# Performance work log

Measured on AMD Instinct MI355X. Metric: run time of the kernel, lower is better.

## Reference

```python
import jax, jax.numpy as jnp
import numpy as np

B, S, D, U, A = 8, 2048, 1024, 1024, 4  # batch, seq, input_dim, units, n_activations


def setup_inputs() -> dict:
    key = jax.random.key(0)
    ks = jax.random.split(key, 6)
    scale_w = (6.0 / (D + U)) ** 0.5  # glorot_uniform
    scale_wf = (6.0 / (U + A)) ** 0.5
    scale_wa = (6.0 / (D + A)) ** 0.5
    return {
        "x": jax.random.normal(ks[0], (B, S, D), dtype=jnp.float32),
        "w": jax.random.uniform(ks[1], (D, U), jnp.float32, -scale_w, scale_w),
        "b": jnp.zeros((U,), jnp.float32),
        "wf": jax.random.uniform(ks[2], (U, A), jnp.float32, -scale_wf, scale_wf),
        "bf": jnp.zeros((U, A), jnp.float32),
        "w_att": jax.random.uniform(ks[3], (D, A), jnp.float32, -scale_wa, scale_wa),
        "b_att": jnp.zeros((A,), jnp.float32),
    }


def reference(x, w, b, wf, bf, w_att, b_att):
    # weighted_sum: [B,S,U]
    ws = jnp.einsum('bsd,du->bsu', x, w) + b
    # broadcast per-activation affine: [B,S,U,A]
    wa = ws[..., None] * wf + bf
    acts = [
        jax.nn.relu(wa[..., 0]),
        jax.nn.sigmoid(wa[..., 1]),
        jnp.tanh(wa[..., 2]),
        jax.nn.gelu(wa[..., 3], approximate=False),  # tf.nn.gelu default is exact
    ]
    result_activations = jnp.stack(acts, axis=-1)  # [B,S,U,A]
    # attention over activations: [B,S,A]
    attn = jax.nn.softmax(jnp.einsum('bsd,da->bsa', x, w_att) + b_att, axis=-1)
    # weighted reduce over activation axis -> [B,S,U]
    out = jnp.einsum('bsua,bsa->bsu', result_activations, attn)
    return out
```

## Files before the change

kernel.cpp:

```cpp
#include <hip/hip_runtime.h>
#include <hip/hip_bf16.h>
#include <cstdint>

#define B_ 8
#define S_ 2048
#define D_ 1024
#define U_ 1024
#define M_ (B_ * S_)

typedef __bf16 bf16x8 __attribute__((ext_vector_type(8)));
typedef float  f32x4  __attribute__((ext_vector_type(4)));

__device__ __forceinline__ uint16_t f2bf(float f) {
  uint32_t u = __builtin_bit_cast(uint32_t, f);
  u += 0x7fffu + ((u >> 16) & 1u);
  return (uint16_t)(u >> 16);
}

__device__ __forceinline__ void async_copy16(const void* g, void* l) {
  typedef const __attribute__((address_space(1))) uint8_t* gp_t;
  typedef __attribute__((address_space(3))) uint8_t* lp_t;
  __builtin_amdgcn_global_load_lds((gp_t)(uintptr_t)g,
                                   (lp_t)(uint32_t)(uintptr_t)l, 16, 0, 0);
}

__global__ __launch_bounds__(256) void k_prep(
    const float* __restrict__ x, const float* __restrict__ w_att,
    const float* __restrict__ b_att, const float* __restrict__ w,
    uint16_t* __restrict__ x_bf, float* __restrict__ attn,
    uint16_t* __restrict__ wt) {
  __shared__ float tile[32][33];
  const int bid = blockIdx.x;
  if (bid < M_ / 4) {
    const int wave = threadIdx.x >> 6, lane = threadIdx.x & 63;
    const int row = bid * 4 + wave;
    const float4* xr = reinterpret_cast<const float4*>(x + (size_t)row * D_);
    const float4* wa4 = reinterpret_cast<const float4*>(w_att);
    float4 v[4];
#pragma unroll
    for (int i = 0; i < 4; i++) v[i] = xr[lane + 64 * i];
    float4 p = {0.f, 0.f, 0.f, 0.f};
#pragma unroll
    for (int i = 0; i < 4; i++) {
      const int base = 4 * (lane + 64 * i);
      const float xe[4] = {v[i].x, v[i].y, v[i].z, v[i].w};
#pragma unroll
      for (int c = 0; c < 4; c++) {
        float4 wv = wa4[base + c];
        p.x = fmaf(xe[c], wv.x, p.x);
        p.y = fmaf(xe[c], wv.y, p.y);
        p.z = fmaf(xe[c], wv.z, p.z);
        p.w = fmaf(xe[c], wv.w, p.w);
      }
      ushort4 hb;
      hb.x = f2bf(v[i].x); hb.y = f2bf(v[i].y);
      hb.z = f2bf(v[i].z); hb.w = f2bf(v[i].w);
      reinterpret_cast<ushort4*>(x_bf + (size_t)row * D_)[lane + 64 * i] = hb;
    }
#pragma unroll
    for (int off = 32; off > 0; off >>= 1) {
      p.x += __shfl_xor(p.x, off);
      p.y += __shfl_xor(p.y, off);
      p.z += __shfl_xor(p.z, off);
      p.w += __shfl_xor(p.w, off);
    }
    if (lane == 0) {
      float l0 = p.x + b_att[0], l1 = p.y + b_att[1];
      float l2 = p.z + b_att[2], l3 = p.w + b_att[3];
      float mx = fmaxf(fmaxf(l0, l1), fmaxf(l2, l3));
      float e0 = __expf(l0 - mx), e1 = __expf(l1 - mx);
      float e2 = __expf(l2 - mx), e3 = __expf(l3 - mx);
      float inv = __builtin_amdgcn_rcpf(e0 + e1 + e2 + e3);
      reinterpret_cast<float4*>(attn)[row] =
          make_float4(e0 * inv, e1 * inv, e2 * inv, e3 * inv);
    }
  } else {
    const int wid = bid - M_ / 4;
    const int t = threadIdx.x;
    const int tx = t & 31, ty = t >> 5;
    const int c0 = (wid & 31) * 32;
    const int r0 = (wid >> 5) * 32;
#pragma unroll
    for (int i = 0; i < 4; i++) {
      int r = ty + i * 8;
      tile[r][tx] = w[(size_t)(r0 + r) * U_ + c0 + tx];
    }
    __syncthreads();
#pragma unroll
    for (int i = 0; i < 4; i++) {
      int r = ty + i * 8;
      wt[(size_t)(c0 + r) * D_ + r0 + tx] = f2bf(tile[tx][r]);
    }
  }
}

#define BM 128
#define BN 128
#define BK 64
#define NXB (U_ / BN)
#define NWG ((M_ / BM) * NXB)

__global__ __launch_bounds__(256, 4) void k_gemm_ep(
    const uint16_t* __restrict__ xbf, const uint16_t* __restrict__ wt,
    const float* __restrict__ bias, const float* __restrict__ wf,
    const float* __restrict__ bfb, const float* __restrict__ attn,
    float* __restrict__ out) {
  __shared__ uint16_t As[BM * BK];
  __shared__ uint16_t Bs[BN * BK];

  const int t = threadIdx.x;
  const int wave = t >> 6, lane = t & 63;
  const int l16 = lane & 15, quad = lane >> 4;
  const int wm = wave >> 1, wn = wave & 1;

  const int h = blockIdx.y * NXB + blockIdx.x;
  const int l = (h & 7) * (NWG / 8) + (h >> 3);
  const int bx = l & (NXB - 1);
  const int by = l / NXB;
  const int m0 = by * BM;
  const int n0 = bx * BN;

  const uint16_t* aBase = xbf + (size_t)m0 * D_;
  const uint16_t* bBase = wt + (size_t)n0 * D_;

  f32x4 acc[4][4] = {};

  for (int k0 = 0; k0 < D_; k0 += BK) {
#pragma unroll
    for (int it = 0; it < 4; it++) {
      int c = t + it * 256;
      int r = c >> 3;
      int cs = c & 7;
      int gc = cs ^ (r & 7);
      async_copy16(aBase + (size_t)r * D_ + k0 + gc * 8, (uint8_t*)As + c * 16);
      async_copy16(bBase + (size_t)r * D_ + k0 + gc * 8, (uint8_t*)Bs + c * 16);
    }
    __syncthreads();

#pragma unroll
    for (int ks = 0; ks < 2; ks++) {
      const int kcb = ks * 4;
      bf16x8 af[4], bfr[4];
#pragma unroll
      for (int i = 0; i < 4; i++) {
        int r = wm * 64 + i * 16 + l16;
        int cs = (kcb + quad) ^ (r & 7);
        af[i] = *reinterpret_cast<const bf16x8*>(&As[r * BK + cs * 8]);
      }
#pragma unroll
      for (int j = 0; j < 4; j++) {
        int n = wn * 64 + j * 16 + l16;
        int cs = (kcb + quad) ^ (n & 7);
        bfr[j] = *reinterpret_cast<const bf16x8*>(&Bs[n * BK + cs * 8]);
      }
#pragma unroll
      for (int i = 0; i < 4; i++)
#pragma unroll
        for (int j = 0; j < 4; j++)
          acc[i][j] = __builtin_amdgcn_mfma_f32_16x16x32_bf16(af[i], bfr[j], acc[i][j], 0, 0, 0);
    }
    __syncthreads();
  }

  float bu[4];
  float4 wf4[4], bf4[4];
#pragma unroll
  for (int j = 0; j < 4; j++) {
    int u = n0 + wn * 64 + j * 16 + l16;
    bu[j] = bias[u];
    wf4[j] = reinterpret_cast<const float4*>(wf)[u];
    bf4[j] = reinterpret_cast<const float4*>(bfb)[u];
  }
#pragma unroll
  for (int i = 0; i < 4; i++) {
#pragma unroll
    for (int r = 0; r < 4; r++) {
      int mg = m0 + wm * 64 + i * 16 + quad * 4 + r;
      float4 at = reinterpret_cast<const float4*>(attn)[mg];
      float* orow = out + (size_t)mg * U_;
#pragma unroll
      for (int j = 0; j < 4; j++) {
        int u = n0 + wn * 64 + j * 16 + l16;
        float wsv = acc[i][j][r] + bu[j];
        float wa0 = fmaf(wsv, wf4[j].x, bf4[j].x);
        float wa1 = fmaf(wsv, wf4[j].y, bf4[j].y);
        float wa2 = fmaf(wsv, wf4[j].z, bf4[j].z);
        float wa3 = fmaf(wsv, wf4[j].w, bf4[j].w);
        float a_relu = fmaxf(wa0, 0.f);
        float a_sig = __builtin_amdgcn_rcpf(
            1.f + __builtin_amdgcn_exp2f(-1.4426950409f * wa1));
        float a_tanh = fmaf(2.f, __builtin_amdgcn_rcpf(
            1.f + __builtin_amdgcn_exp2f(-2.8853900818f * wa2)), -1.f);
        float y = wa3 * fmaf(0.044715f, wa3 * wa3, 1.f);
        float a_gelu = wa3 * __builtin_amdgcn_rcpf(
            1.f + __builtin_amdgcn_exp2f(-2.302207929f * y));
        float res = at.x * a_relu + at.y * a_sig + at.z * a_tanh + at.w * a_gelu;
        __builtin_nontemporal_store(res, &orow[u]);
      }
    }
  }
}

extern "C" void kernel_launch(void* const* d_in, const int* in_sizes, int n_in,
                              void* d_out, int out_size, void* d_ws, size_t ws_size,
                              hipStream_t stream) {
  const float* x     = (const float*)d_in[0];
  const float* w     = (const float*)d_in[1];
  const float* b     = (const float*)d_in[2];
  const float* wf    = (const float*)d_in[3];
  const float* bfb   = (const float*)d_in[4];
  const float* w_att = (const float*)d_in[5];
  const float* b_att = (const float*)d_in[6];
  float* out = (float*)d_out;

  char* ws = (char*)d_ws;
  uint16_t* x_bf = (uint16_t*)ws;
  uint16_t* w_t  = (uint16_t*)(ws + ((size_t)32 << 20));
  float*    attn = (float*)(ws + ((size_t)34 << 20));

  k_prep<<<dim3(M_ / 4 + 1024), 256, 0, stream>>>(x, w_att, b_att, w, x_bf, attn, w_t);
  k_gemm_ep<<<dim3(U_ / BN, M_ / BM), 256, 0, stream>>>(x_bf, w_t, b, wf, bfb, attn, out);
}
```

Before: 173.8 us.

## Fuse x bf16 conversion and attention logits into GEMM A-tile loads

Drops the prep pass that wrote a bf16 copy of x and the attention softmax to workspace. The GEMM now loads fp32 x directly, converts it to bf16 in registers before storing to LDS, and accumulates the attention logits during the k-loop, finishing the softmax in shared memory. This removes a full read/write pass over x and one kernel's worth of traffic. In exchange, each of the 8 column blocks re-reads fp32 x (twice the bytes of bf16), the A loads become synchronous instead of async-to-LDS, and the attention dot product is recomputed once per column block. The output store is also changed from nontemporal to a normal store.

```diff
diff --git a/kernel.cpp b/kernel.cpp
--- a/kernel.cpp
+++ b/kernel.cpp
@@ -24,73 +24,24 @@
                                    (lp_t)(uint32_t)(uintptr_t)l, 16, 0, 0);
 }
 
-__global__ __launch_bounds__(256) void k_prep(
-    const float* __restrict__ x, const float* __restrict__ w_att,
-    const float* __restrict__ b_att, const float* __restrict__ w,
-    uint16_t* __restrict__ x_bf, float* __restrict__ attn,
-    uint16_t* __restrict__ wt) {
+__global__ __launch_bounds__(256) void k_tr(
+    const float* __restrict__ w, uint16_t* __restrict__ wt) {
   __shared__ float tile[32][33];
-  const int bid = blockIdx.x;
-  if (bid < M_ / 4) {
-    const int wave = threadIdx.x >> 6, lane = threadIdx.x & 63;
-    const int row = bid * 4 + wave;
-    const float4* xr = reinterpret_cast<const float4*>(x + (size_t)row * D_);
-    const float4* wa4 = reinterpret_cast<const float4*>(w_att);
-    float4 v[4];
-#pragma unroll
-    for (int i = 0; i < 4; i++) v[i] = xr[lane + 64 * i];
-    float4 p = {0.f, 0.f, 0.f, 0.f};
-#pragma unroll
-    for (int i = 0; i < 4; i++) {
-      const int base = 4 * (lane + 64 * i);
-      const float xe[4] = {v[i].x, v[i].y, v[i].z, v[i].w};
-#pragma unroll
-      for (int c = 0; c < 4; c++) {
-        float4 wv = wa4[base + c];
-        p.x = fmaf(xe[c], wv.x, p.x);
-        p.y = fmaf(xe[c], wv.y, p.y);
-        p.z = fmaf(xe[c], wv.z, p.z);
-        p.w = fmaf(xe[c], wv.w, p.w);
-      }
-      ushort4 hb;
-      hb.x = f2bf(v[i].x); hb.y = f2bf(v[i].y);
-      hb.z = f2bf(v[i].z); hb.w = f2bf(v[i].w);
-      reinterpret_cast<ushort4*>(x_bf + (size_t)row * D_)[lane + 64 * i] = hb;
-    }
-#pragma unroll
-    for (int off = 32; off > 0; off >>= 1) {
-      p.x += __shfl_xor(p.x, off);
-      p.y += __shfl_xor(p.y, off);
-      p.z += __shfl_xor(p.z, off);
-      p.w += __shfl_xor(p.w, off);
-    }
-    if (lane == 0) {
-      float l0 = p.x + b_att[0], l1 = p.y + b_att[1];
-      float l2 = p.z + b_att[2], l3 = p.w + b_att[3];
-      float mx = fmaxf(fmaxf(l0, l1), fmaxf(l2, l3));
-      float e0 = __expf(l0 - mx), e1 = __expf(l1 - mx);
-      float e2 = __expf(l2 - mx), e3 = __expf(l3 - mx);
-      float inv = __builtin_amdgcn_rcpf(e0 + e1 + e2 + e3);
-      reinterpret_cast<float4*>(attn)[row] =
-          make_float4(e0 * inv, e1 * inv, e2 * inv, e3 * inv);
-    }
-  } else {
-    const int wid = bid - M_ / 4;
-    const int t = threadIdx.x;
-    const int tx = t & 31, ty = t >> 5;
-    const int c0 = (wid & 31) * 32;
-    const int r0 = (wid >> 5) * 32;
-#pragma unroll
-    for (int i = 0; i < 4; i++) {
-      int r = ty + i * 8;
-      tile[r][tx] = w[(size_t)(r0 + r) * U_ + c0 + tx];
-    }
-    __syncthreads();
-#pragma unroll
-    for (int i = 0; i < 4; i++) {
-      int r = ty + i * 8;
-      wt[(size_t)(c0 + r) * D_ + r0 + tx] = f2bf(tile[tx][r]);
-    }
+  const int wid = blockIdx.x;
+  const int t = threadIdx.x;
+  const int tx = t & 31, ty = t >> 5;
+  const int c0 = (wid & 31) * 32;
+  const int r0 = (wid >> 5) * 32;
+#pragma unroll
+  for (int i = 0; i < 4; i++) {
+    int r = ty + i * 8;
+    tile[r][tx] = w[(size_t)(r0 + r) * U_ + c0 + tx];
+  }
+  __syncthreads();
+#pragma unroll
+  for (int i = 0; i < 4; i++) {
+    int r = ty + i * 8;
+    wt[(size_t)(c0 + r) * D_ + r0 + tx] = f2bf(tile[tx][r]);
   }
 }
 
@@ -100,13 +51,14 @@
 #define NXB (U_ / BN)
 #define NWG ((M_ / BM) * NXB)
 
-__global__ __launch_bounds__(256, 4) void k_gemm_ep(
-    const uint16_t* __restrict__ xbf, const uint16_t* __restrict__ wt,
+__global__ __launch_bounds__(256, 4) void k_gemm_f(
+    const float* __restrict__ x, const uint16_t* __restrict__ wt,
     const float* __restrict__ bias, const float* __restrict__ wf,
-    const float* __restrict__ bfb, const float* __restrict__ attn,
-    float* __restrict__ out) {
+    const float* __restrict__ bfb, const float* __restrict__ w_att,
+    const float* __restrict__ b_att, float* __restrict__ out) {
   __shared__ uint16_t As[BM * BK];
   __shared__ uint16_t Bs[BN * BK];
+  __shared__ float4 attn_s[BM];
 
   const int t = threadIdx.x;
   const int wave = t >> 6, lane = t & 63;
@@ -120,20 +72,45 @@
   const int m0 = by * BM;
   const int n0 = bx * BN;
 
-  const uint16_t* aBase = xbf + (size_t)m0 * D_;
   const uint16_t* bBase = wt + (size_t)n0 * D_;
+  const float4* wa4 = reinterpret_cast<const float4*>(w_att);
 
   f32x4 acc[4][4] = {};
+  float4 patt[4] = {};
 
   for (int k0 = 0; k0 < D_; k0 += BK) {
 #pragma unroll
     for (int it = 0; it < 4; it++) {
       int c = t + it * 256;
       int r = c >> 3;
-      int cs = c & 7;
-      int gc = cs ^ (r & 7);
-      async_copy16(aBase + (size_t)r * D_ + k0 + gc * 8, (uint8_t*)As + c * 16);
+      int gc = (c & 7) ^ (r & 7);
       async_copy16(bBase + (size_t)r * D_ + k0 + gc * 8, (uint8_t*)Bs + c * 16);
+    }
+#pragma unroll
+    for (int it = 0; it < 4; it++) {
+      int c = t + it * 256;
+      int r = c >> 3;
+      int gc = (c & 7) ^ (r & 7);
+      const float* g = x + (size_t)(m0 + r) * D_ + k0 + gc * 8;
+      float4 lo = *reinterpret_cast<const float4*>(g);
+      float4 hi = *reinterpret_cast<const float4*>(g + 4);
+      const float4* wrow = wa4 + k0 + gc * 8;
+      float4 pa = patt[it];
+#define ACC4(val, wv) do { float4 _w = (wv);                        \
+        pa.x = fmaf((val), _w.x, pa.x); pa.y = fmaf((val), _w.y, pa.y); \
+        pa.z = fmaf((val), _w.z, pa.z); pa.w = fmaf((val), _w.w, pa.w); } while (0)
+      ACC4(lo.x, wrow[0]); ACC4(lo.y, wrow[1]);
+      ACC4(lo.z, wrow[2]); ACC4(lo.w, wrow[3]);
+      ACC4(hi.x, wrow[4]); ACC4(hi.y, wrow[5]);
+      ACC4(hi.z, wrow[6]); ACC4(hi.w, wrow[7]);
+#undef ACC4
+      patt[it] = pa;
+      bf16x8 hb;
+      hb[0] = (__bf16)lo.x; hb[1] = (__bf16)lo.y;
+      hb[2] = (__bf16)lo.z; hb[3] = (__bf16)lo.w;
+      hb[4] = (__bf16)hi.x; hb[5] = (__bf16)hi.y;
+      hb[6] = (__bf16)hi.z; hb[7] = (__bf16)hi.w;
+      *reinterpret_cast<bf16x8*>((uint8_t*)As + c * 16) = hb;
     }
     __syncthreads();
 
@@ -162,6 +139,28 @@
     __syncthreads();
   }
 
+#pragma unroll
+  for (int it = 0; it < 4; it++) {
+    float4 pa = patt[it];
+#pragma unroll
+    for (int off = 1; off <= 4; off <<= 1) {
+      pa.x += __shfl_xor(pa.x, off);
+      pa.y += __shfl_xor(pa.y, off);
+      pa.z += __shfl_xor(pa.z, off);
+      pa.w += __shfl_xor(pa.w, off);
+    }
+    if ((t & 7) == 0) {
+      float l0 = pa.x + b_att[0], l1 = pa.y + b_att[1];
+      float l2 = pa.z + b_att[2], l3 = pa.w + b_att[3];
+      float mx = fmaxf(fmaxf(l0, l1), fmaxf(l2, l3));
+      float e0 = __expf(l0 - mx), e1 = __expf(l1 - mx);
+      float e2 = __expf(l2 - mx), e3 = __expf(l3 - mx);
+      float inv = __builtin_amdgcn_rcpf(e0 + e1 + e2 + e3);
+      attn_s[(t >> 3) + it * 32] = make_float4(e0 * inv, e1 * inv, e2 * inv, e3 * inv);
+    }
+  }
+  __syncthreads();
+
   float bu[4];
   float4 wf4[4], bf4[4];
 #pragma unroll
@@ -175,9 +174,9 @@
   for (int i = 0; i < 4; i++) {
 #pragma unroll
     for (int r = 0; r < 4; r++) {
-      int mg = m0 + wm * 64 + i * 16 + quad * 4 + r;
-      float4 at = reinterpret_cast<const float4*>(attn)[mg];
-      float* orow = out + (size_t)mg * U_;
+      int ml = wm * 64 + i * 16 + quad * 4 + r;
+      float4 at = attn_s[ml];
+      float* orow = out + (size_t)(m0 + ml) * U_;
 #pragma unroll
       for (int j = 0; j < 4; j++) {
         int u = n0 + wn * 64 + j * 16 + l16;
@@ -194,8 +193,7 @@
         float y = wa3 * fmaf(0.044715f, wa3 * wa3, 1.f);
         float a_gelu = wa3 * __builtin_amdgcn_rcpf(
             1.f + __builtin_amdgcn_exp2f(-2.302207929f * y));
-        float res = at.x * a_relu + at.y * a_sig + at.z * a_tanh + at.w * a_gelu;
-        __builtin_nontemporal_store(res, &orow[u]);
+        orow[u] = at.x * a_relu + at.y * a_sig + at.z * a_tanh + at.w * a_gelu;
       }
     }
   }
@@ -214,10 +212,9 @@
   float* out = (float*)d_out;
 
   char* ws = (char*)d_ws;
-  uint16_t* x_bf = (uint16_t*)ws;
-  uint16_t* w_t  = (uint16_t*)(ws + ((size_t)32 << 20));
-  float*    attn = (float*)(ws + ((size_t)34 << 20));
-
-  k_prep<<<dim3(M_ / 4 + 1024), 256, 0, stream>>>(x, w_att, b_att, w, x_bf, attn, w_t);
-  k_gemm_ep<<<dim3(U_ / BN, M_ / BM), 256, 0, stream>>>(x_bf, w_t, b, wf, bfb, attn, out);
-}
+  uint16_t* w_t = (uint16_t*)ws;
+
+  k_tr<<<dim3(1024), 256, 0, stream>>>(w, w_t);
+  k_gemm_f<<<dim3(U_ / BN, M_ / BM), 256, 0, stream>>>(
+      x, w_t, b, wf, bfb, w_att, b_att, out);
+}
```

New measurement: 442.5 us. 2.55x slower.
